# Kernel tuning notes

Hardware: AMD Instinct MI355X
Metric: run time of the kernel (lower is better)

Reference implementation:

```python
import jax, jax.numpy as jnp
import numpy as np

B, RULE_DIM, E, P, TOP_K = 8192, 128, 64, 16, 3
EPS = 1e-5
CONF_THRESH = 0.1


def _ln(x, g, b):
    # torch.nn.LayerNorm: biased variance, eps=1e-5
    m = x.mean(-1, keepdims=True)
    v = ((x - m) ** 2).mean(-1, keepdims=True)
    return (x - m) / jnp.sqrt(v + EPS) * g + b


def setup_inputs() -> dict:
    key = jax.random.key(0)
    ks = jax.random.split(key, 8)
    s = lambda fan: 1.0 / np.sqrt(fan)
    return {
        "rule_embedding": jax.random.normal(ks[0], (B, RULE_DIM), jnp.float32),
        "rp_w1": jax.random.normal(ks[1], (RULE_DIM, 256), jnp.float32) * s(RULE_DIM),
        "rp_b1": jnp.zeros((256,), jnp.float32),
        "rp_g1": jnp.ones((256,), jnp.float32),
        "rp_be1": jnp.zeros((256,), jnp.float32),
        "rp_w2": jax.random.normal(ks[2], (256, 512), jnp.float32) * s(256),
        "rp_b2": jnp.zeros((512,), jnp.float32),
        "rp_g2": jnp.ones((512,), jnp.float32),
        "rp_be2": jnp.zeros((512,), jnp.float32),
        "op_w": jax.random.normal(ks[3], (512, E), jnp.float32) * s(512),
        "op_b": jnp.zeros((E,), jnp.float32),
        "pe_w1": jax.random.normal(ks[4], (E, 512, 256), jnp.float32) * s(512),
        "pe_b1": jnp.zeros((E, 256), jnp.float32),
        "pe_g": jnp.ones((E, 256), jnp.float32),
        "pe_beta": jnp.zeros((E, 256), jnp.float32),
        "pe_w2": jax.random.normal(ks[5], (E, 256, P), jnp.float32) * s(256),
        "pe_b2": jnp.zeros((E, P), jnp.float32),
    }


def reference(rule_embedding, rp_w1, rp_b1, rp_g1, rp_be1, rp_w2, rp_b2,
              rp_g2, rp_be2, op_w, op_b, pe_w1, pe_b1, pe_g, pe_beta,
              pe_w2, pe_b2):
    # rule_parser: Linear -> LN -> ReLU -> Linear -> LN -> ReLU
    h = jax.nn.relu(_ln(rule_embedding @ rp_w1 + rp_b1, rp_g1, rp_be1))   # [B,256]
    features = jax.nn.relu(_ln(h @ rp_w2 + rp_b2, rp_g2, rp_be2))         # [B,512]

    # op routing: softmax + top-k
    op_probs = jax.nn.softmax(features @ op_w + op_b, axis=-1)            # [B,E]
    top_probs, top_idx = jax.lax.top_k(op_probs, TOP_K)                   # [B,K]

    # per-op param predictor MLP, evaluated for every expert (vmap over E)
    def expert(w1, b1, g, be, w2, b2):
        z = jax.nn.relu(_ln(features @ w1 + b1, g, be))                   # [B,256]
        return z @ w2 + b2                                                # [B,P]

    h2_all = jax.vmap(expert)(pe_w1, pe_b1, pe_g, pe_beta, pe_w2, pe_b2)  # [E,B,P]

    # gather the selected expert's raw param logits per (token, slot)
    params_sel = h2_all[top_idx, jnp.arange(B)[:, None], :]               # [B,K,P]

    # original skips ops with confidence < 0.1 -> mask them out
    mask = (top_probs >= CONF_THRESH).astype(params_sel.dtype)            # [B,K]
    params_out = params_sel * mask[..., None]

    return top_probs, top_idx, params_out
```

## Files before the change

### kernel.cpp

```cpp
#include <hip/hip_runtime.h>
#include <math.h>

#define Bv   8192
#define EPSv 1e-5f
#define CONFv 0.1f
#define MB (1024*1024)

typedef __attribute__((ext_vector_type(8))) short short8;
typedef __attribute__((ext_vector_type(4))) float f32x4;

__device__ __forceinline__ float wave_sum64(float v){
  #pragma unroll
  for (int o = 32; o; o >>= 1) v += __shfl_xor(v, o, 64);
  return v;
}

__device__ __forceinline__ void split3f(float x, short &h, short &m, short &l){
  unsigned u = __float_as_uint(x);
  h = (short)(u >> 16);
  float r1 = x - __uint_as_float(u & 0xffff0000u);
  unsigned u1 = __float_as_uint(r1);
  m = (short)(u1 >> 16);
  float r2 = r1 - __uint_as_float(u1 & 0xffff0000u);
  l = (short)(__float_as_uint(r2) >> 16);
}

__device__ __forceinline__ f32x4 mfma6(short8 ah, short8 am, short8 al,
                                       short8 bh, short8 bm, short8 bl, f32x4 c){
  c = __builtin_amdgcn_mfma_f32_16x16x32_bf16(al, bh, c, 0, 0, 0);
  c = __builtin_amdgcn_mfma_f32_16x16x32_bf16(ah, bl, c, 0, 0, 0);
  c = __builtin_amdgcn_mfma_f32_16x16x32_bf16(am, bm, c, 0, 0, 0);
  c = __builtin_amdgcn_mfma_f32_16x16x32_bf16(am, bh, c, 0, 0, 0);
  c = __builtin_amdgcn_mfma_f32_16x16x32_bf16(ah, bm, c, 0, 0, 0);
  c = __builtin_amdgcn_mfma_f32_16x16x32_bf16(ah, bh, c, 0, 0, 0);
  return c;
}

__device__ __forceinline__ f32x4 mfma5(short8 ah, short8 am,
                                       short8 bh, short8 bm, short8 bl, f32x4 c){
  c = __builtin_amdgcn_mfma_f32_16x16x32_bf16(am, bm, c, 0, 0, 0);
  c = __builtin_amdgcn_mfma_f32_16x16x32_bf16(ah, bl, c, 0, 0, 0);
  c = __builtin_amdgcn_mfma_f32_16x16x32_bf16(am, bh, c, 0, 0, 0);
  c = __builtin_amdgcn_mfma_f32_16x16x32_bf16(ah, bm, c, 0, 0, 0);
  c = __builtin_amdgcn_mfma_f32_16x16x32_bf16(ah, bh, c, 0, 0, 0);
  return c;
}

__device__ __forceinline__ f32x4 mfma3(short8 ah, short8 al,
                                       short8 bh, short8 bl, f32x4 c){
  c = __builtin_amdgcn_mfma_f32_16x16x32_bf16(al, bh, c, 0, 0, 0);
  c = __builtin_amdgcn_mfma_f32_16x16x32_bf16(ah, bl, c, 0, 0, 0);
  c = __builtin_amdgcn_mfma_f32_16x16x32_bf16(ah, bh, c, 0, 0, 0);
  return c;
}

__global__ __launch_bounds__(256) void k_pack(const float* __restrict__ pw1,
    const float* __restrict__ pw2, const float* __restrict__ w1,
    const float* __restrict__ w2, const float* __restrict__ opw,
    unsigned short* __restrict__ p1, unsigned short* __restrict__ p2,
    unsigned short* __restrict__ w1p, unsigned short* __restrict__ w2p,
    unsigned short* __restrict__ opwp, int* __restrict__ cnt)
{
  int bid = blockIdx.x;
  if (bid < 4096){
    int t = bid*256 + threadIdx.x;
    int e = t >> 14, rem = t & 16383, kg = rem >> 8, n = rem & 255;
    const float* src = pw1 + ((size_t)e << 17) + (size_t)(kg*8)*256 + n;
    short8 h, l;
    #pragma unroll
    for (int j = 0; j < 8; j++){
      float w = src[(size_t)j*256];
      unsigned u = __float_as_uint(w);
      float r2 = w - __uint_as_float(u & 0xffff0000u);
      h[j] = (short)(u >> 16);
      l[j] = (short)(__float_as_uint(r2) >> 16);
    }
    int idx8 = ((((n >> 4)*16 + (kg >> 2))*64) + (kg & 3)*16 + (n & 15)) << 3;
    unsigned short* ep = p1 + (size_t)e * 262144;
    *(short8*)(ep + idx8)          = h;
    *(short8*)(ep + 131072 + idx8) = l;
  } else if (bid < 4224){
    int t = (bid - 4096)*256 + threadIdx.x;
    int e = t >> 9, rem = t & 511, kg = rem >> 4, n = rem & 15;
    const float* src = pw2 + (size_t)e*4096 + (size_t)(kg*8)*16 + n;
    short8 h, l;
    #pragma unroll
    for (int j = 0; j < 8; j++){
      float w = src[(size_t)j*16];
      unsigned u = __float_as_uint(w);
      float r2 = w - __uint_as_float(u & 0xffff0000u);
      h[j] = (short)(u >> 16);
      l[j] = (short)(__float_as_uint(r2) >> 16);
    }
    int idx8 = (((kg >> 2)*64) + (kg & 3)*16 + n) << 3;
    unsigned short* ep = p2 + (size_t)e * 8192;
    *(short8*)(ep + idx8)        = h;
    *(short8*)(ep + 4096 + idx8) = l;
  } else if (bid < 4352){
    int gid = (bid - 4224)*256 + threadIdx.x;
    int k = gid >> 8, n = gid & 255;
    short h, m, l;
    split3f(w1[gid], h, m, l);
    int idx = (((n >> 4)*4 + (k >> 5))*64 + (((k >> 3) & 3)*16 + (n & 15)))*8 + (k & 7);
    w1p[idx]             = (unsigned short)h;
    w1p[32768 + idx]     = (unsigned short)m;
    w1p[2*32768 + idx]   = (unsigned short)l;
  } else if (bid < 4864){
    int gid = (bid - 4352)*256 + threadIdx.x;
    int k = gid >> 9, n = gid & 511;
    short h, m, l;
    split3f(w2[gid], h, m, l);
    int idx = (((n >> 4)*8 + (k >> 5))*64 + (((k >> 3) & 3)*16 + (n & 15)))*8 + (k & 7);
    w2p[idx]             = (unsigned short)h;
    w2p[131072 + idx]    = (unsigned short)m;
    w2p[2*131072 + idx]  = (unsigned short)l;
  } else if (bid < 4992){
    int gid = (bid - 4864)*256 + threadIdx.x;
    int k = gid >> 6, n = gid & 63;
    short h, m, l;
    split3f(opw[gid], h, m, l);
    int idx = (((n >> 4)*16 + (k >> 5))*64 + (((k >> 3) & 3)*16 + (n & 15)))*8 + (k & 7);
    opwp[idx]            = (unsigned short)h;
    opwp[32768 + idx]    = (unsigned short)m;
    opwp[2*32768 + idx]  = (unsigned short)l;
  } else {
    if (threadIdx.x < 64) cnt[threadIdx.x] = 0;
  }
}

__global__ __launch_bounds__(512) void k_fused(const float* __restrict__ X,
    const unsigned short* __restrict__ w1p, const float* __restrict__ b1,
    const float* __restrict__ g1, const float* __restrict__ be1,
    const unsigned short* __restrict__ w2p, const float* __restrict__ b2,
    const float* __restrict__ g2, const float* __restrict__ be2,
    const unsigned short* __restrict__ opwp, const float* __restrict__ opb,
    unsigned short* __restrict__ fh, unsigned short* __restrict__ fl,
    float* __restrict__ dout, int* __restrict__ cnt, int* __restrict__ list)
{
  extern __shared__ unsigned char smem[];
  float*          xs = (float*)smem;
  unsigned short* hb = (unsigned short*)(smem + 16384);
  unsigned short* ga = (unsigned short*)smem;
  __shared__ float part[8][32][2];
  __shared__ float lg[32][64];

  const int tid = threadIdx.x;
  const int r0  = blockIdx.x * 32;
  const int wave = tid >> 6, lane = tid & 63, lquad = lane >> 4, l15 = lane & 15;

  for (int i = tid; i < 32*32; i += 512){
    int r = i >> 5, c4 = i & 31;
    float4 v = ((const float4*)X)[(size_t)(r0+r)*32 + c4];
    int off = r*128 + (((c4 >> 1) ^ (r & 7)) << 3) + ((c4 & 1) << 2);
    *(float4*)(xs + off) = v;
  }
  __syncthreads();

  {
    f32x4 acc[2][2];
    #pragma unroll
    for (int mt = 0; mt < 2; mt++)
      #pragma unroll
      for (int nt = 0; nt < 2; nt++) acc[mt][nt] = (f32x4){0.f,0.f,0.f,0.f};
    const int pstride = 32768;
    for (int ks4 = 0; ks4 < 4; ks4++){
      short8 ah[2], am[2], al[2];
      #pragma unroll
      for (int mt = 0; mt < 2; mt++){
        int r = mt*16 + l15;
        const float* ap = xs + r*128 + (((ks4*4 + lquad) ^ (r & 7)) << 3);
        float4 a0 = *(const float4*)ap;
        float4 a1 = *(const float4*)(ap + 4);
        float av[8] = {a0.x,a0.y,a0.z,a0.w,a1.x,a1.y,a1.z,a1.w};
        #pragma unroll
        for (int j = 0; j < 8; j++){
          short hh, mm2, ll;
          split3f(av[j], hh, mm2, ll);
          ah[mt][j] = hh; am[mt][j] = mm2; al[mt][j] = ll;
        }
      }
      #pragma unroll
      for (int nt = 0; nt < 2; nt++){
        int ntg = wave*2 + nt;
        const unsigned short* bp = w1p + (size_t)(((ntg*4 + ks4)*64 + lane)*8);
        short8 bh = *(const short8*)bp;
        short8 bm = *(const short8*)(bp + pstride);
        short8 bl = *(const short8*)(bp + 2*pstride);
        #pragma unroll
        for (int mt = 0; mt < 2; mt++)
          acc[mt][nt] = mfma6(ah[mt], am[mt], al[mt], bh, bm, bl, acc[mt][nt]);
      }
    }
    float bcol[2], gcol[2], becol[2];
    #pragma unroll
    for (int nt = 0; nt < 2; nt++){
      int col = (wave*2 + nt)*16 + l15;
      bcol[nt] = b1[col]; gcol[nt] = g1[col]; becol[nt] = be1[col];
    }
    #pragma unroll
    for (int mt = 0; mt < 2; mt++)
      #pragma unroll
      for (int reg = 0; reg < 4; reg++){
        float s = 0.f, q = 0.f;
        #pragma unroll
        for (int nt = 0; nt < 2; nt++){
          float z = acc[mt][nt][reg] + bcol[nt];
          s += z; q += z*z;
        }
        #pragma unroll
        for (int o = 1; o < 16; o <<= 1){ s += __shfl_xor(s, o, 64); q += __shfl_xor(q, o, 64); }
        int row = mt*16 + lquad*4 + reg;
        if (l15 == 0){ part[wave][row][0] = s; part[wave][row][1] = q; }
      }
    __syncthreads();
    #pragma unroll
    for (int mt = 0; mt < 2; mt++)
      #pragma unroll
      for (int reg = 0; reg < 4; reg++){
        int row = mt*16 + lquad*4 + reg;
        float s = 0.f, q = 0.f;
        #pragma unroll
        for (int w8 = 0; w8 < 8; w8++){ s += part[w8][row][0]; q += part[w8][row][1]; }
        float mean = s * (1.0f/256.0f);
        float var  = q * (1.0f/256.0f) - mean*mean;
        float inv  = 1.0f / sqrtf(var + EPSv);
        #pragma unroll
        for (int nt = 0; nt < 2; nt++){
          int col = (wave*2 + nt)*16 + l15;
          float z = acc[mt][nt][reg] + bcol[nt];
          float y = fmaxf((z - mean)*inv*gcol[nt] + becol[nt], 0.f);
          short hh, mm2, ll;
          split3f(y, hh, mm2, ll);
          int gg = col >> 3, c7 = col & 7;
          int adr = row*256 + ((gg ^ (row & 7)) << 3) + c7;
          hb[adr]         = (unsigned short)hh;
          hb[8192 + adr]  = (unsigned short)mm2;
          hb[16384 + adr] = (unsigned short)ll;
        }
      }
  }
  __syncthreads();

  f32x4 acc2[2][4];
  #pragma unroll
  for (int mt = 0; mt < 2; mt++)
    #pragma unroll
    for (int nt = 0; nt < 4; nt++) acc2[mt][nt] = (f32x4){0.f,0.f,0.f,0.f};
  {
    const int pstride = 131072;
    for (int ks4 = 0; ks4 < 8; ks4++){
      short8 ah[2], am[2], al[2];
      #pragma unroll
      for (int mt = 0; mt < 2; mt++){
        int r = mt*16 + l15;
        int goff = r*256 + (((ks4*4 + lquad) ^ (r & 7)) << 3);
        ah[mt] = *(const short8*)(hb + goff);
        am[mt] = *(const short8*)(hb + 8192 + goff);
        al[mt] = *(const short8*)(hb + 16384 + goff);
      }
      #pragma unroll
      for (int nt = 0; nt < 4; nt++){
        int ntg = wave*4 + nt;
        const unsigned short* bp = w2p + (size_t)(((ntg*8 + ks4)*64 + lane)*8);
        short8 bh = *(const short8*)bp;
        short8 bm = *(const short8*)(bp + pstride);
        short8 bl = *(const short8*)(bp + 2*pstride);
        #pragma unroll
        for (int mt = 0; mt < 2; mt++)
          acc2[mt][nt] = mfma6(ah[mt], am[mt], al[mt], bh, bm, bl, acc2[mt][nt]);
      }
    }
  }

  float bcol[4], gcol[4], becol[4];
  #pragma unroll
  for (int nt = 0; nt < 4; nt++){
    int col = (wave*4 + nt)*16 + l15;
    bcol[nt] = b2[col]; gcol[nt] = g2[col]; becol[nt] = be2[col];
  }
  #pragma unroll
  for (int mt = 0; mt < 2; mt++)
    #pragma unroll
    for (int reg = 0; reg < 4; reg++){
      float s = 0.f, q = 0.f;
      #pragma unroll
      for (int nt = 0; nt < 4; nt++){
        float z = acc2[mt][nt][reg] + bcol[nt];
        s += z; q += z*z;
      }
      #pragma unroll
      for (int o = 1; o < 16; o <<= 1){ s += __shfl_xor(s, o, 64); q += __shfl_xor(q, o, 64); }
      int row = mt*16 + lquad*4 + reg;
      if (l15 == 0){ part[wave][row][0] = s; part[wave][row][1] = q; }
    }
  __syncthreads();

  #pragma unroll
  for (int mt = 0; mt < 2; mt++)
    #pragma unroll
    for (int reg = 0; reg < 4; reg++){
      int row = mt*16 + lquad*4 + reg;
      float s = 0.f, q = 0.f;
      #pragma unroll
      for (int w8 = 0; w8 < 8; w8++){ s += part[w8][row][0]; q += part[w8][row][1]; }
      float mean = s * (1.0f/512.0f);
      float var  = q * (1.0f/512.0f) - mean*mean;
      float inv  = 1.0f / sqrtf(var + EPSv);
      #pragma unroll
      for (int nt = 0; nt < 4; nt++){
        int col = (wave*4 + nt)*16 + l15;
        float z = acc2[mt][nt][reg] + bcol[nt];
        float y = fmaxf((z - mean)*inv*gcol[nt] + becol[nt], 0.f);
        short hh, mm2, ll;
        split3f(y, hh, mm2, ll);
        int gg = col >> 3, c7 = col & 7;
        int adr = row*512 + ((gg ^ (row & 7)) << 3) + c7;
        ga[adr]          = (unsigned short)hh;
        ga[16384 + adr]  = (unsigned short)mm2;
      }
    }
  __syncthreads();

  if (wave < 4){
    f32x4 accg[2];
    accg[0] = (f32x4){0.f,0.f,0.f,0.f};
    accg[1] = (f32x4){0.f,0.f,0.f,0.f};
    for (int kt = 0; kt < 16; kt++){
      const unsigned short* bp = opwp + (((wave*16 + kt)*64 + lane) << 3);
      short8 bh = *(const short8*)bp;
      short8 bm = *(const short8*)(bp + 32768);
      short8 bl = *(const short8*)(bp + 65536);
      #pragma unroll
      for (int mt = 0; mt < 2; mt++){
        int r = mt*16 + l15;
        int off = r*512 + (((kt*4 + lquad) ^ (r & 7)) << 3);
        short8 ah = *(const short8*)(ga + off);
        short8 am = *(const short8*)(ga + 16384 + off);
        accg[mt] = mfma5(ah, am, bh, bm, bl, accg[mt]);
      }
    }
    float opbv = opb[wave*16 + l15];
    #pragma unroll
    for (int mt = 0; mt < 2; mt++)
      #pragma unroll
      for (int reg = 0; reg < 4; reg++)
        lg[mt*16 + lquad*4 + reg][wave*16 + l15] = accg[mt][reg] + opbv;
  } else {
    int t4 = (wave - 4)*64 + lane;
    for (int i = t4; i < 4096; i += 256){
      int p = i >> 11, rem = i & 2047, r = rem >> 6, gg = rem & 63;
      short8 v = *(const short8*)(ga + p*16384 + r*512 + ((gg ^ (r & 7)) << 3));
      unsigned short* dst = (p ? fl : fh) + (size_t)(r0 + r)*512 + gg*8;
      *(short8*)dst = v;
    }
  }
  __syncthreads();

  {
    for (int rr = 0; rr < 4; rr++){
      int r = wave*4 + rr, row = r0 + r;
      float l = lg[r][lane];
      float mx = l;
      #pragma unroll
      for (int o = 32; o; o >>= 1) mx = fmaxf(mx, __shfl_xor(mx, o, 64));
      float p = expf(l - mx);
      float s = wave_sum64(p);
      p /= s;
      float pv = p;
      for (int j = 0; j < 3; j++){
        float v = pv; int idx = lane;
        #pragma unroll
        for (int o = 32; o; o >>= 1){
          float ov = __shfl_xor(v, o, 64);
          int   oi = __shfl_xor(idx, o, 64);
          if (ov > v || (ov == v && oi < idx)){ v = ov; idx = oi; }
        }
        if (lane == 0){
          dout[(size_t)row*3 + j]                = v;
          dout[(size_t)Bv*3 + (size_t)row*3 + j] = (float)idx;
        }
        if (v >= CONFv){
          if (lane == 0){
            int pos = atomicAdd(&cnt[idx], 1);
            list[idx*Bv + pos] = (row << 2) | j;
          }
        } else {
          if (lane < 16) dout[(size_t)Bv*6 + (size_t)row*48 + j*16 + lane] = 0.f;
        }
        if (lane == idx) pv = -1.0f;
      }
    }
  }
}

__global__ __launch_bounds__(256) void k_expert(const unsigned short* __restrict__ fh,
    const unsigned short* __restrict__ fl,
    const unsigned short* __restrict__ p1, const float* __restrict__ b1,
    const float* __restrict__ g,  const float* __restrict__ beta,
    const unsigned short* __restrict__ p2, const float* __restrict__ b2,
    const int* __restrict__ cnt,  const int* __restrict__ list,
    float* __restrict__ dout)
{
  extern __shared__ unsigned char smem[];
  unsigned short* xh = (unsigned short*)smem;
  unsigned short* xl = xh + 32*512;
  float*          zs = (float*)smem;
  unsigned short* zp = (unsigned short*)smem;
  __shared__ int sdesc[3];

  const int tid = threadIdx.x;
  const int wave = tid >> 6, lane = tid & 63;
  const int lquad = lane >> 4, l15 = lane & 15;

  if (wave == 0){
    int c  = cnt[lane];
    int tl = (c + 31) >> 5;
    int incl = tl;
    #pragma unroll
    for (int o = 1; o < 64; o <<= 1){
      int v = __shfl_up(incl, o, 64);
      if (lane >= o) incl += v;
    }
    int total = __shfl(incl, 63, 64);
    int G   = (total + 7) >> 3;
    int grp = blockIdx.x & 7, rr = blockIdx.x >> 3;
    int lgc = grp*G + rr;
    int ok  = (G > 0) && (rr < G) && (lgc < total);
    unsigned long long bm = __ballot(ok && (incl > lgc));
    if (lane == 0){
      if (!ok || bm == 0ull){ sdesc[0] = -1; }
      else {
        int e = __ffsll((long long)bm) - 1;
        sdesc[0] = e; sdesc[1] = lgc; sdesc[2] = 0;
      }
    }
    if (bm != 0ull && ok){
      int e = __ffsll((long long)bm) - 1;
      int excl = __shfl(incl - tl, e, 64);
      int ne   = __shfl(c, e, 64);
      if (lane == 0){ sdesc[1] = lgc - excl; sdesc[2] = ne; }
    }
  }
  __syncthreads();
  const int e = sdesc[0];
  if (e < 0) return;
  const int t = sdesc[1];
  const int n = sdesc[2];
  const int base = t * 32;
  const int m = min(32, n - base);
  const int* lrow = list + e*Bv + base;

  for (int i = tid; i < 4096; i += 256){
    int p = i >> 11, rem = i & 2047, r = rem >> 6, gg = rem & 63;
    int ev = lrow[(r < m) ? r : 0];
    int row = ev >> 2;
    const unsigned short* src = (p ? fl : fh) + (size_t)row*512 + gg*8;
    short8 v = *(const short8*)src;
    unsigned short* dst = (p ? xl : xh) + r*512 + ((gg ^ (r & 7)) << 3);
    *(short8*)dst = v;
  }
  __syncthreads();

  const unsigned short* p1e = p1 + (size_t)e * 262144;
  const int colbase = wave * 64;
  f32x4 acc[2][4];
  #pragma unroll
  for (int mt = 0; mt < 2; mt++)
    #pragma unroll
    for (int nt = 0; nt < 4; nt++) acc[mt][nt] = (f32x4){0.f,0.f,0.f,0.f};

  for (int kt = 0; kt < 16; kt++){
    short8 ah[2], al[2];
    int gk = kt*4 + lquad;
    #pragma unroll
    for (int mt = 0; mt < 2; mt++){
      int r = mt*16 + l15;
      int off = r*512 + ((gk ^ (r & 7)) << 3);
      ah[mt] = *(const short8*)(xh + off);
      al[mt] = *(const short8*)(xl + off);
    }
    #pragma unroll
    for (int nt = 0; nt < 4; nt++){
      int ntg = wave*4 + nt;
      const unsigned short* bp = p1e + (((ntg*16 + kt)*64 + lane) << 3);
      short8 bh = *(const short8*)bp;
      short8 bl = *(const short8*)(bp + 131072);
      #pragma unroll
      for (int mt = 0; mt < 2; mt++)
        acc[mt][nt] = mfma3(ah[mt], al[mt], bh, bl, acc[mt][nt]);
    }
  }
  __syncthreads();

  #pragma unroll
  for (int nt = 0; nt < 4; nt++){
    int col = colbase + nt*16 + l15;
    float bb = b1[e*256 + col];
    #pragma unroll
    for (int mt = 0; mt < 2; mt++)
      #pragma unroll
      for (int rg = 0; rg < 4; rg++){
        int rl = mt*16 + lquad*4 + rg;
        zs[rl*264 + col] = acc[mt][nt][rg] + bb;
      }
  }
  __syncthreads();

  {
    float gv[4], bv[4];
    #pragma unroll
    for (int j = 0; j < 4; j++){
      gv[j] = g[e*256 + lane + 64*j];
      bv[j] = beta[e*256 + lane + 64*j];
    }
    for (int rr2 = 0; rr2 < 8; rr2++){
      int r = wave*8 + rr2;
      float x[4];
      float s = 0.f;
      #pragma unroll
      for (int j = 0; j < 4; j++){ x[j] = zs[r*264 + lane + 64*j]; s += x[j]; }
      s = wave_sum64(s);
      float mm = s * (1.0f/256.0f);
      float v = 0.f;
      #pragma unroll
      for (int j = 0; j < 4; j++){ float d = x[j] - mm; v += d*d; }
      v = wave_sum64(v) * (1.0f/256.0f);
      float inv = 1.0f / sqrtf(v + EPSv);
      #pragma unroll
      for (int j = 0; j < 4; j++){
        int c = lane + 64*j;
        float y = fmaxf((x[j] - mm)*inv*gv[j] + bv[j], 0.f);
        unsigned u = __float_as_uint(y);
        float res = y - __uint_as_float(u & 0xffff0000u);
        zp[r*528 + c]       = (unsigned short)(u >> 16);
        zp[r*528 + 264 + c] = (unsigned short)(__float_as_uint(res) >> 16);
      }
    }
  }
  __syncthreads();

  if (wave < 2){
    const unsigned short* p2e = p2 + (size_t)e * 8192;
    f32x4 acc2 = (f32x4){0.f,0.f,0.f,0.f};
    for (int kt2 = 0; kt2 < 8; kt2++){
      const unsigned short* zb = zp + (wave*16 + l15)*528 + kt2*32 + lquad*8;
      short8 ahh = *(const short8*)zb;
      short8 all2 = *(const short8*)(zb + 264);
      const unsigned short* bp = p2e + ((kt2*64 + lane) << 3);
      short8 bh = *(const short8*)bp;
      short8 bl = *(const short8*)(bp + 4096);
      acc2 = mfma3(ahh, all2, bh, bl, acc2);
    }
    float b2v = b2[e*16 + l15];
    #pragma unroll
    for (int reg = 0; reg < 4; reg++){
      int rl = wave*16 + lquad*4 + reg;
      if (rl < m){
        int ev = lrow[rl];
        int row = ev >> 2, j = ev & 3;
        dout[(size_t)Bv*6 + (size_t)row*48 + j*16 + l15] = acc2[reg] + b2v;
      }
    }
  }
}

extern "C" void kernel_launch(void* const* d_in, const int* in_sizes, int n_in,
                              void* d_out, int out_size, void* d_ws, size_t ws_size,
                              hipStream_t stream)
{
  const float* X   = (const float*)d_in[0];
  const float* w1  = (const float*)d_in[1];
  const float* b1  = (const float*)d_in[2];
  const float* g1  = (const float*)d_in[3];
  const float* be1 = (const float*)d_in[4];
  const float* w2  = (const float*)d_in[5];
  const float* b2  = (const float*)d_in[6];
  const float* g2  = (const float*)d_in[7];
  const float* be2 = (const float*)d_in[8];
  const float* opw = (const float*)d_in[9];
  const float* opb = (const float*)d_in[10];
  const float* pw1 = (const float*)d_in[11];
  const float* pb1 = (const float*)d_in[12];
  const float* pg  = (const float*)d_in[13];
  const float* pbe = (const float*)d_in[14];
  const float* pw2 = (const float*)d_in[15];
  const float* pb2 = (const float*)d_in[16];
  float* out = (float*)d_out;
  char*  ws  = (char*)d_ws;

  unsigned short* p1E    = (unsigned short*)ws;
  unsigned short* p2E    = (unsigned short*)(ws + (size_t)32*MB);
  unsigned short* w1p_rp = (unsigned short*)(ws + (size_t)33*MB);
  unsigned short* w2p_rp = (unsigned short*)(ws + (size_t)34*MB);
  unsigned short* opwp   = (unsigned short*)(ws + (size_t)35*MB);
  unsigned short* fh     = (unsigned short*)(ws + (size_t)36*MB);
  unsigned short* fl     = (unsigned short*)(ws + (size_t)44*MB);
  int*            list   = (int*)(ws + (size_t)52*MB);
  int*            cnt    = (int*)(ws + (size_t)54*MB);

  k_pack  <<<4993, 256, 0, stream>>>(pw1, pw2, w1, w2, opw, p1E, p2E,
                                     w1p_rp, w2p_rp, opwp, cnt);
  k_fused <<<256,  512, 65536, stream>>>(X, w1p_rp, b1, g1, be1,
                                         w2p_rp, b2, g2, be2, opwp, opb,
                                         fh, fl, out, cnt, list);
  k_expert<<<832,  256, 65536, stream>>>(fh, fl, p1E, pb1, pg, pbe, p2E, pb2,
                                         cnt, list, out);
}
```

Baseline: 183.1 us.

## Double waves in fused rule-parser kernel and use two-way activation splits

The fused rule-parser kernel now launches 1024 threads per block instead of 512, so each wave handles half as many output column tiles in both MLP layers and half as many rows in the softmax/top-k stage. Activations are now split into bf16 hi/mid parts only: the input X is pre-split once into shared memory, and the 6-MFMA products become 5-MFMA products, dropping the low activation part. This cuts MFMA count, conversion work and shared-memory traffic in exchange for slightly lower precision, plus more waves per block competing for registers.

```diff
diff --git a/kernel.cpp b/kernel.cpp
--- a/kernel.cpp
+++ b/kernel.cpp
@@ -25,15 +25,11 @@
   l = (short)(__float_as_uint(r2) >> 16);
 }
 
-__device__ __forceinline__ f32x4 mfma6(short8 ah, short8 am, short8 al,
-                                       short8 bh, short8 bm, short8 bl, f32x4 c){
-  c = __builtin_amdgcn_mfma_f32_16x16x32_bf16(al, bh, c, 0, 0, 0);
-  c = __builtin_amdgcn_mfma_f32_16x16x32_bf16(ah, bl, c, 0, 0, 0);
-  c = __builtin_amdgcn_mfma_f32_16x16x32_bf16(am, bm, c, 0, 0, 0);
-  c = __builtin_amdgcn_mfma_f32_16x16x32_bf16(am, bh, c, 0, 0, 0);
-  c = __builtin_amdgcn_mfma_f32_16x16x32_bf16(ah, bm, c, 0, 0, 0);
-  c = __builtin_amdgcn_mfma_f32_16x16x32_bf16(ah, bh, c, 0, 0, 0);
-  return c;
+__device__ __forceinline__ void split2f(float x, short &h, short &m){
+  unsigned u = __float_as_uint(x);
+  h = (short)(u >> 16);
+  float r1 = x - __uint_as_float(u & 0xffff0000u);
+  m = (short)(__float_as_uint(r1) >> 16);
 }
 
 __device__ __forceinline__ f32x4 mfma5(short8 ah, short8 am,
@@ -128,7 +124,7 @@
   }
 }
 
-__global__ __launch_bounds__(512) void k_fused(const float* __restrict__ X,
+__global__ __launch_bounds__(1024) void k_fused(const float* __restrict__ X,
     const unsigned short* __restrict__ w1p, const float* __restrict__ b1,
     const float* __restrict__ g1, const float* __restrict__ be1,
     const unsigned short* __restrict__ w2p, const float* __restrict__ b2,
@@ -138,144 +134,135 @@
     float* __restrict__ dout, int* __restrict__ cnt, int* __restrict__ list)
 {
   extern __shared__ unsigned char smem[];
-  float*          xs = (float*)smem;
-  unsigned short* hb = (unsigned short*)(smem + 16384);
-  unsigned short* ga = (unsigned short*)smem;
-  __shared__ float part[8][32][2];
+  unsigned short* xh  = (unsigned short*)smem;
+  unsigned short* xm  = xh + 4096;
+  unsigned short* hbh = xh + 8192;
+  unsigned short* hbm = xh + 16384;
+  unsigned short* gah = xh;
+  unsigned short* gam = xh + 16384;
+  __shared__ float part[16][32][2];
   __shared__ float lg[32][64];
 
   const int tid = threadIdx.x;
   const int r0  = blockIdx.x * 32;
   const int wave = tid >> 6, lane = tid & 63, lquad = lane >> 4, l15 = lane & 15;
 
-  for (int i = tid; i < 32*32; i += 512){
-    int r = i >> 5, c4 = i & 31;
+  {
+    int r = tid >> 5, c4 = tid & 31;
     float4 v = ((const float4*)X)[(size_t)(r0+r)*32 + c4];
-    int off = r*128 + (((c4 >> 1) ^ (r & 7)) << 3) + ((c4 & 1) << 2);
-    *(float4*)(xs + off) = v;
-  }
-  __syncthreads();
-
+    unsigned u0 = __float_as_uint(v.x), u1 = __float_as_uint(v.y);
+    unsigned u2 = __float_as_uint(v.z), u3 = __float_as_uint(v.w);
+    float m0 = v.x - __uint_as_float(u0 & 0xffff0000u);
+    float m1 = v.y - __uint_as_float(u1 & 0xffff0000u);
+    float m2 = v.z - __uint_as_float(u2 & 0xffff0000u);
+    float m3 = v.w - __uint_as_float(u3 & 0xffff0000u);
+    unsigned hp0 = (u0 >> 16) | (u1 & 0xffff0000u);
+    unsigned hp1 = (u2 >> 16) | (u3 & 0xffff0000u);
+    unsigned mp0 = (__float_as_uint(m0) >> 16) | (__float_as_uint(m1) & 0xffff0000u);
+    unsigned mp1 = (__float_as_uint(m2) >> 16) | (__float_as_uint(m3) & 0xffff0000u);
+    int gk = c4 >> 1, half = c4 & 1;
+    int off = r*128 + ((gk ^ (r & 7)) << 3) + half*4;
+    ((unsigned*)(xh + off))[0] = hp0;
+    ((unsigned*)(xh + off))[1] = hp1;
+    ((unsigned*)(xm + off))[0] = mp0;
+    ((unsigned*)(xm + off))[1] = mp1;
+  }
+  __syncthreads();
+
+  float bcol1, gcol1, becol1;
   {
-    f32x4 acc[2][2];
-    #pragma unroll
-    for (int mt = 0; mt < 2; mt++)
-      #pragma unroll
-      for (int nt = 0; nt < 2; nt++) acc[mt][nt] = (f32x4){0.f,0.f,0.f,0.f};
+    int col = wave*16 + l15;
+    bcol1 = b1[col]; gcol1 = g1[col]; becol1 = be1[col];
+  }
+  {
+    f32x4 acc[2];
+    acc[0] = (f32x4){0.f,0.f,0.f,0.f};
+    acc[1] = (f32x4){0.f,0.f,0.f,0.f};
     const int pstride = 32768;
     for (int ks4 = 0; ks4 < 4; ks4++){
-      short8 ah[2], am[2], al[2];
+      const unsigned short* bp = w1p + (((wave*4 + ks4)*64 + lane) << 3);
+      short8 bh = *(const short8*)bp;
+      short8 bm = *(const short8*)(bp + pstride);
+      short8 bl = *(const short8*)(bp + 2*pstride);
       #pragma unroll
       for (int mt = 0; mt < 2; mt++){
         int r = mt*16 + l15;
-        const float* ap = xs + r*128 + (((ks4*4 + lquad) ^ (r & 7)) << 3);
-        float4 a0 = *(const float4*)ap;
-        float4 a1 = *(const float4*)(ap + 4);
-        float av[8] = {a0.x,a0.y,a0.z,a0.w,a1.x,a1.y,a1.z,a1.w};
+        int off = r*128 + (((ks4*4 + lquad) ^ (r & 7)) << 3);
+        short8 ah = *(const short8*)(xh + off);
+        short8 am = *(const short8*)(xm + off);
+        acc[mt] = mfma5(ah, am, bh, bm, bl, acc[mt]);
+      }
+    }
+    #pragma unroll
+    for (int mt = 0; mt < 2; mt++)
+      #pragma unroll
+      for (int reg = 0; reg < 4; reg++){
+        float z = acc[mt][reg] + bcol1;
+        float s = z, q = z*z;
         #pragma unroll
-        for (int j = 0; j < 8; j++){
-          short hh, mm2, ll;
-          split3f(av[j], hh, mm2, ll);
-          ah[mt][j] = hh; am[mt][j] = mm2; al[mt][j] = ll;
-        }
+        for (int o = 1; o < 16; o <<= 1){ s += __shfl_xor(s, o, 64); q += __shfl_xor(q, o, 64); }
+        int row = mt*16 + lquad*4 + reg;
+        if (l15 == 0){ part[wave][row][0] = s; part[wave][row][1] = q; }
+      }
+    __syncthreads();
+    #pragma unroll
+    for (int mt = 0; mt < 2; mt++)
+      #pragma unroll
+      for (int reg = 0; reg < 4; reg++){
+        int row = mt*16 + lquad*4 + reg;
+        float s = 0.f, q = 0.f;
+        #pragma unroll
+        for (int w16 = 0; w16 < 16; w16++){ s += part[w16][row][0]; q += part[w16][row][1]; }
+        float mean = s * (1.0f/256.0f);
+        float var  = q * (1.0f/256.0f) - mean*mean;
+        float inv  = 1.0f / sqrtf(var + EPSv);
+        int col = wave*16 + l15;
+        float z = acc[mt][reg] + bcol1;
+        float y = fmaxf((z - mean)*inv*gcol1 + becol1, 0.f);
+        short hh, mm2;
+        split2f(y, hh, mm2);
+        int gg = col >> 3, c7 = col & 7;
+        int adr = row*256 + ((gg ^ (row & 7)) << 3) + c7;
+        hbh[adr] = (unsigned short)hh;
+        hbm[adr] = (unsigned short)mm2;
+      }
+  }
+  __syncthreads();
+
+  f32x4 acc2[2][2];
+  #pragma unroll
+  for (int mt = 0; mt < 2; mt++)
+    #pragma unroll
+    for (int nt = 0; nt < 2; nt++) acc2[mt][nt] = (f32x4){0.f,0.f,0.f,0.f};
+  {
+    const int pstride = 131072;
+    for (int ks4 = 0; ks4 < 8; ks4++){
+      short8 ah[2], am[2];
+      #pragma unroll
+      for (int mt = 0; mt < 2; mt++){
+        int r = mt*16 + l15;
+        int off = r*256 + (((ks4*4 + lquad) ^ (r & 7)) << 3);
+        ah[mt] = *(const short8*)(hbh + off);
+        am[mt] = *(const short8*)(hbm + off);
       }
       #pragma unroll
       for (int nt = 0; nt < 2; nt++){
         int ntg = wave*2 + nt;
-        const unsigned short* bp = w1p + (size_t)(((ntg*4 + ks4)*64 + lane)*8);
+        const unsigned short* bp = w2p + (((ntg*8 + ks4)*64 + lane) << 3);
         short8 bh = *(const short8*)bp;
         short8 bm = *(const short8*)(bp + pstride);
         short8 bl = *(const short8*)(bp + 2*pstride);
         #pragma unroll
         for (int mt = 0; mt < 2; mt++)
-          acc[mt][nt] = mfma6(ah[mt], am[mt], al[mt], bh, bm, bl, acc[mt][nt]);
-      }
-    }
-    float bcol[2], gcol[2], becol[2];
-    #pragma unroll
-    for (int nt = 0; nt < 2; nt++){
-      int col = (wave*2 + nt)*16 + l15;
-      bcol[nt] = b1[col]; gcol[nt] = g1[col]; becol[nt] = be1[col];
-    }
-    #pragma unroll
-    for (int mt = 0; mt < 2; mt++)
-      #pragma unroll
-      for (int reg = 0; reg < 4; reg++){
-        float s = 0.f, q = 0.f;
-        #pragma unroll
-        for (int nt = 0; nt < 2; nt++){
-          float z = acc[mt][nt][reg] + bcol[nt];
-          s += z; q += z*z;
-        }
-        #pragma unroll
-        for (int o = 1; o < 16; o <<= 1){ s += __shfl_xor(s, o, 64); q += __shfl_xor(q, o, 64); }
-        int row = mt*16 + lquad*4 + reg;
-        if (l15 == 0){ part[wave][row][0] = s; part[wave][row][1] = q; }
-      }
-    __syncthreads();
-    #pragma unroll
-    for (int mt = 0; mt < 2; mt++)
-      #pragma unroll
-      for (int reg = 0; reg < 4; reg++){
-        int row = mt*16 + lquad*4 + reg;
-        float s = 0.f, q = 0.f;
-        #pragma unroll
-        for (int w8 = 0; w8 < 8; w8++){ s += part[w8][row][0]; q += part[w8][row][1]; }
-        float mean = s * (1.0f/256.0f);
-        float var  = q * (1.0f/256.0f) - mean*mean;
-        float inv  = 1.0f / sqrtf(var + EPSv);
-        #pragma unroll
-        for (int nt = 0; nt < 2; nt++){
-          int col = (wave*2 + nt)*16 + l15;
-          float z = acc[mt][nt][reg] + bcol[nt];
-          float y = fmaxf((z - mean)*inv*gcol[nt] + becol[nt], 0.f);
-          short hh, mm2, ll;
-          split3f(y, hh, mm2, ll);
-          int gg = col >> 3, c7 = col & 7;
-          int adr = row*256 + ((gg ^ (row & 7)) << 3) + c7;
-          hb[adr]         = (unsigned short)hh;
-          hb[8192 + adr]  = (unsigned short)mm2;
-          hb[16384 + adr] = (unsigned short)ll;
-        }
-      }
-  }
-  __syncthreads();
-
-  f32x4 acc2[2][4];
-  #pragma unroll
-  for (int mt = 0; mt < 2; mt++)
-    #pragma unroll
-    for (int nt = 0; nt < 4; nt++) acc2[mt][nt] = (f32x4){0.f,0.f,0.f,0.f};
-  {
-    const int pstride = 131072;
-    for (int ks4 = 0; ks4 < 8; ks4++){
-      short8 ah[2], am[2], al[2];
-      #pragma unroll
-      for (int mt = 0; mt < 2; mt++){
-        int r = mt*16 + l15;
-        int goff = r*256 + (((ks4*4 + lquad) ^ (r & 7)) << 3);
-        ah[mt] = *(const short8*)(hb + goff);
-        am[mt] = *(const short8*)(hb + 8192 + goff);
-        al[mt] = *(const short8*)(hb + 16384 + goff);
-      }
-      #pragma unroll
-      for (int nt = 0; nt < 4; nt++){
-        int ntg = wave*4 + nt;
-        const unsigned short* bp = w2p + (size_t)(((ntg*8 + ks4)*64 + lane)*8);
-        short8 bh = *(const short8*)bp;
-        short8 bm = *(const short8*)(bp + pstride);
-        short8 bl = *(const short8*)(bp + 2*pstride);
-        #pragma unroll
-        for (int mt = 0; mt < 2; mt++)
-          acc2[mt][nt] = mfma6(ah[mt], am[mt], al[mt], bh, bm, bl, acc2[mt][nt]);
-      }
-    }
-  }
-
-  float bcol[4], gcol[4], becol[4];
-  #pragma unroll
-  for (int nt = 0; nt < 4; nt++){
-    int col = (wave*4 + nt)*16 + l15;
+          acc2[mt][nt] = mfma5(ah[mt], am[mt], bh, bm, bl, acc2[mt][nt]);
+      }
+    }
+  }
+
+  float bcol[2], gcol[2], becol[2];
+  #pragma unroll
+  for (int nt = 0; nt < 2; nt++){
+    int col = (wave*2 + nt)*16 + l15;
     bcol[nt] = b2[col]; gcol[nt] = g2[col]; becol[nt] = be2[col];
   }
   #pragma unroll
@@ -284,7 +271,7 @@
     for (int reg = 0; reg < 4; reg++){
       float s = 0.f, q = 0.f;
       #pragma unroll
-      for (int nt = 0; nt < 4; nt++){
+      for (int nt = 0; nt < 2; nt++){
         float z = acc2[mt][nt][reg] + bcol[nt];
         s += z; q += z*z;
       }
@@ -302,21 +289,21 @@
       int row = mt*16 + lquad*4 + reg;
       float s = 0.f, q = 0.f;
       #pragma unroll
-      for (int w8 = 0; w8 < 8; w8++){ s += part[w8][row][0]; q += part[w8][row][1]; }
+      for (int w16 = 0; w16 < 16; w16++){ s += part[w16][row][0]; q += part[w16][row][1]; }
       float mean = s * (1.0f/512.0f);
       float var  = q * (1.0f/512.0f) - mean*mean;
       float inv  = 1.0f / sqrtf(var + EPSv);
       #pragma unroll
-      for (int nt = 0; nt < 4; nt++){
-        int col = (wave*4 + nt)*16 + l15;
+      for (int nt = 0; nt < 2; nt++){
+        int col = (wave*2 + nt)*16 + l15;
         float z = acc2[mt][nt][reg] + bcol[nt];
         float y = fmaxf((z - mean)*inv*gcol[nt] + becol[nt], 0.f);
-        short hh, mm2, ll;
-        split3f(y, hh, mm2, ll);
+        short hh, mm2;
+        split2f(y, hh, mm2);
         int gg = col >> 3, c7 = col & 7;
         int adr = row*512 + ((gg ^ (row & 7)) << 3) + c7;
-        ga[adr]          = (unsigned short)hh;
-        ga[16384 + adr]  = (unsigned short)mm2;
+        gah[adr] = (unsigned short)hh;
+        gam[adr] = (unsigned short)mm2;
       }
     }
   __syncthreads();
@@ -334,8 +321,8 @@
       for (int mt = 0; mt < 2; mt++){
         int r = mt*16 + l15;
         int off = r*512 + (((kt*4 + lquad) ^ (r & 7)) << 3);
-        short8 ah = *(const short8*)(ga + off);
-        short8 am = *(const short8*)(ga + 16384 + off);
+        short8 ah = *(const short8*)(gah + off);
+        short8 am = *(const short8*)(gam + off);
         accg[mt] = mfma5(ah, am, bh, bm, bl, accg[mt]);
       }
     }
@@ -347,9 +334,9 @@
         lg[mt*16 + lquad*4 + reg][wave*16 + l15] = accg[mt][reg] + opbv;
   } else {
     int t4 = (wave - 4)*64 + lane;
-    for (int i = t4; i < 4096; i += 256){
+    for (int i = t4; i < 4096; i += 768){
       int p = i >> 11, rem = i & 2047, r = rem >> 6, gg = rem & 63;
-      short8 v = *(const short8*)(ga + p*16384 + r*512 + ((gg ^ (r & 7)) << 3));
+      short8 v = *(const short8*)((p ? gam : gah) + r*512 + ((gg ^ (r & 7)) << 3));
       unsigned short* dst = (p ? fl : fh) + (size_t)(r0 + r)*512 + gg*8;
       *(short8*)dst = v;
     }
@@ -357,8 +344,8 @@
   __syncthreads();
 
   {
-    for (int rr = 0; rr < 4; rr++){
-      int r = wave*4 + rr, row = r0 + r;
+    for (int rr = 0; rr < 2; rr++){
+      int r = wave*2 + rr, row = r0 + r;
       float l = lg[r][lane];
       float mx = l;
       #pragma unroll
@@ -600,7 +587,7 @@
 
   k_pack  <<<4993, 256, 0, stream>>>(pw1, pw2, w1, w2, opw, p1E, p2E,
                                      w1p_rp, w2p_rp, opwp, cnt);
-  k_fused <<<256,  512, 65536, stream>>>(X, w1p_rp, b1, g1, be1,
+  k_fused <<<256, 1024, 65536, stream>>>(X, w1p_rp, b1, g1, be1,
                                          w2p_rp, b2, g2, be2, opwp, opb,
                                          fh, fl, out, cnt, list);
   k_expert<<<832,  256, 65536, stream>>>(fh, fl, p1E, pb1, pg, pbe, p2E, pb2,
```

Result: no change. 179.9 us (-1.7%).
